# Optimization experiments

Hardware: AMD Instinct MI355X
Metric: run time of the kernel (lower is better)

## Reference

```python
import jax, jax.numpy as jnp
import numpy as np

WS = 7   # window_size
NH = 4   # num_head
EPS = 1e-5

def _rel_idx(ws):
    c = np.stack(np.meshgrid(np.arange(ws), np.arange(ws), indexing='ij')).reshape(2, -1)
    r = (c[:, :, None] - c[:, None, :]).transpose(1, 2, 0)
    r[..., 0] += ws - 1
    r[..., 1] += ws - 1
    r[..., 0] *= 2 * ws - 1
    return r.sum(-1)  # (ws^2, ws^2) int

def _shift_mask(ws, ps):
    # faithful to torch get_shift_mask: additive mask value is (1-eq)*1e-9 (as in source)
    wn = ps // ws
    ss = ws // 2
    rt = (np.arange(ps) + ss) // ws
    m = rt[:, None] * (ps // ws) + rt[None, :] + 1
    m = np.roll(m, (-ss, -ss), axis=(0, 1))
    m = m.reshape(wn, ws, wn, ws).transpose(0, 2, 1, 3).reshape(wn * wn, ws * ws)
    eq = (m[:, :, None] == m[:, None, :]).astype(np.float32)
    return (1.0 - eq) * 1e-9  # (num_windows, ws^2, ws^2)

def _ln(x, g, b):
    mu = x.mean(-1, keepdims=True)
    v = ((x - mu) ** 2).mean(-1, keepdims=True)
    return (x - mu) * jax.lax.rsqrt(v + EPS) * g + b

def _win_attn(x, wqkv, bqkv, wo, bo, table, mask):
    bs, S, D = x.shape
    hd = D // NH
    qkv = x @ wqkv.T + bqkv
    q, k, v = jnp.split(qkv, 3, axis=-1)
    def heads(t):
        return t.reshape(bs, S, NH, hd).transpose(0, 2, 1, 3).reshape(bs * NH, S, hd)
    q, k, v = heads(q), heads(k), heads(v)
    ridx = _rel_idx(WS).reshape(-1)
    bias = table[ridx].reshape(S, S, NH).transpose(2, 0, 1)  # (NH, S, S)
    scores = jnp.einsum('bqd,bkd->bqk', q, k) / np.sqrt(hd).astype(np.float32)
    scores = scores + jnp.tile(bias, (bs, 1, 1))
    if mask is not None:
        # source tiles mask head-major while q/k/v are batch-major; replicate faithfully
        scores = scores + jnp.tile(mask, (NH, 1, 1))
    p = jax.nn.softmax(scores, axis=-1)
    out = jnp.einsum('bqk,bkd->bqd', p, v)
    out = out.reshape(bs, NH, S, hd).transpose(0, 2, 1, 3).reshape(bs, S, D)
    return out @ wo.T + bo

def _forward(x, ln1_g, ln1_b, w_qkv1, b_qkv1, w_o1, b_o1, tbl1,
             ln2_g, ln2_b, w_mlp1, b_mlp1,
             ln3_g, ln3_b, w_qkv2, b_qkv2, w_o2, b_o2, tbl2,
             ln4_g, ln4_b, w_mlp2, b_mlp2):
    B, S, D = x.shape
    ps = int(np.sqrt(S))
    wn = ps // WS
    nw = wn * wn
    s2 = WS * WS
    ss = WS // 2
    # block 1: W-MSA (note: source's image2sequence is a plain reshape, no inverse transpose)
    y = _ln(x, ln1_g, ln1_b)
    y = y.reshape(B, wn, WS, wn, WS, D).transpose(0, 1, 3, 2, 4, 5).reshape(B * nw, s2, D)
    y = _win_attn(y, w_qkv1, b_qkv1, w_o1, b_o1, tbl1, None)
    y = y.reshape(B, S, D)
    x = x + y
    # mlp1
    y = _ln(x, ln2_g, ln2_b) @ w_mlp1.T + b_mlp1
    x = x + y
    # block 2: SW-MSA
    y = _ln(x, ln3_g, ln3_b)
    y = jnp.roll(y.reshape(B, ps, ps, D), (-ss, -ss), axis=(1, 2))
    y = y.reshape(B, wn, WS, wn, WS, D).transpose(0, 1, 3, 2, 4, 5).reshape(B * nw, s2, D)
    mask = jnp.tile(jnp.asarray(_shift_mask(WS, ps)), (B, 1, 1))
    y = _win_attn(y, w_qkv2, b_qkv2, w_o2, b_o2, tbl2, mask)
    y = y.reshape(B, wn, wn, WS, WS, D).transpose(0, 1, 3, 2, 4, 5).reshape(B, ps, ps, D)
    y = jnp.roll(y, (ss, ss), axis=(1, 2)).reshape(B, S, D)
    x = x + y
    # mlp2; source line `y + x + y` has no assignment, so the final residual is dropped
    y = _ln(x, ln4_g, ln4_b) @ w_mlp2.T + b_mlp2
    return y

def setup_inputs() -> dict:
    key = jax.random.key(0)
    ks = jax.random.split(key, 16)
    B, S, D = 64, 3136, 128
    T = (2 * WS - 1) ** 2  # 169
    f32 = jnp.float32
    inp = {
        'x': jax.random.normal(ks[0], (B, S, D), dtype=f32),
        'ln1_g': jnp.ones((D,), f32), 'ln1_b': jnp.zeros((D,), f32),
        'w_qkv1': jax.random.normal(ks[1], (3 * D, D), dtype=f32) * 0.02,
        'b_qkv1': jnp.zeros((3 * D,), f32),
        'w_o1': jax.random.normal(ks[2], (D, D), dtype=f32) * 0.02,
        'b_o1': jnp.zeros((D,), f32),
        'tbl1': jax.random.normal(ks[3], (T, NH), dtype=f32) * 0.02,
        'ln2_g': jnp.ones((D,), f32), 'ln2_b': jnp.zeros((D,), f32),
        'w_mlp1': jax.random.normal(ks[4], (D, D), dtype=f32) * 0.02,
        'b_mlp1': jnp.zeros((D,), f32),
        'ln3_g': jnp.ones((D,), f32), 'ln3_b': jnp.zeros((D,), f32),
        'w_qkv2': jax.random.normal(ks[5], (3 * D, D), dtype=f32) * 0.02,
        'b_qkv2': jnp.zeros((3 * D,), f32),
        'w_o2': jax.random.normal(ks[6], (D, D), dtype=f32) * 0.02,
        'b_o2': jnp.zeros((D,), f32),
        'tbl2': jax.random.normal(ks[7], (T, NH), dtype=f32) * 0.02,
        'ln4_g': jnp.ones((D,), f32), 'ln4_b': jnp.zeros((D,), f32),
        'w_mlp2': jax.random.normal(ks[8], (D, D), dtype=f32) * 0.02,
        'b_mlp2': jnp.zeros((D,), f32),
    }
    return inp

def reference(x, ln1_g, ln1_b, w_qkv1, b_qkv1, w_o1, b_o1, tbl1,
              ln2_g, ln2_b, w_mlp1, b_mlp1,
              ln3_g, ln3_b, w_qkv2, b_qkv2, w_o2, b_o2, tbl2,
              ln4_g, ln4_b, w_mlp2, b_mlp2):
    return _forward(x, ln1_g, ln1_b, w_qkv1, b_qkv1, w_o1, b_o1, tbl1,
                    ln2_g, ln2_b, w_mlp1, b_mlp1,
                    ln3_g, ln3_b, w_qkv2, b_qkv2, w_o2, b_o2, tbl2,
                    ln4_g, ln4_b, w_mlp2, b_mlp2)
```

## Files before the change

### kernel.cpp

```cpp
#include <hip/hip_runtime.h>
#include <hip/hip_bf16.h>
#include <stdint.h>

#define PS 56
#define S_ 3136
#define DIM 128
#define NTOK 200704

typedef __attribute__((ext_vector_type(8))) short short8;
typedef __attribute__((ext_vector_type(4))) float f32x4;

__device__ __forceinline__ float bflo(uint32_t u){ return __uint_as_float(u << 16); }
__device__ __forceinline__ float bfhi(uint32_t u){ return __uint_as_float(u & 0xffff0000u); }
__device__ __forceinline__ uint32_t bfpack(float a, float b){
  uint32_t ua = __float_as_uint(a); ua = (ua + 0x7fffu + ((ua >> 16) & 1u)) >> 16;
  uint32_t ub = __float_as_uint(b); ub = (ub + 0x7fffu + ((ub >> 16) & 1u)) & 0xffff0000u;
  return ua | ub;
}
__device__ __forceinline__ uint16_t bf16of(float a){
  uint32_t ua = __float_as_uint(a);
  return (uint16_t)((ua + 0x7fffu + ((ua >> 16) & 1u)) >> 16);
}

__device__ __forceinline__ int win_map(int r, int shift) {
  int b = r / S_;
  int rem = r - b * S_;
  int w = rem / 49;
  int p = rem - w * 49;
  int i = p / 7, j = p - i * 7;
  int wr = w >> 3, wc = w & 7;
  int row = wr * 7 + i + shift; if (row >= PS) row -= PS;
  int col = wc * 7 + j + shift; if (col >= PS) col -= PS;
  return b * S_ + row * PS + col;
}

__global__ __launch_bounds__(256) void ln_k(const float* __restrict__ X,
                                            const float* __restrict__ g,
                                            const float* __restrict__ b,
                                            uint16_t* __restrict__ O) {
  int t = blockIdx.x * 4 + (threadIdx.x >> 6);
  int lane = threadIdx.x & 63;
  float2 v = *(const float2*)(X + (size_t)t * DIM + lane * 2);
  float s = v.x + v.y, sq = v.x * v.x + v.y * v.y;
  #pragma unroll
  for (int o = 32; o; o >>= 1) { s += __shfl_xor(s, o); sq += __shfl_xor(sq, o); }
  float mu = s * (1.0f / 128.0f);
  float rs = rsqrtf(sq * (1.0f / 128.0f) - mu * mu + 1e-5f);
  float2 gg = *(const float2*)(g + lane * 2);
  float2 bb = *(const float2*)(b + lane * 2);
  float a = (v.x - mu) * rs * gg.x + bb.x;
  float c = (v.y - mu) * rs * gg.y + bb.y;
  ((uint32_t*)O)[(size_t)t * 64 + lane] = bfpack(a, c);
}

__global__ __launch_bounds__(256) void wconv_k(
    const float* __restrict__ w0, const float* __restrict__ w1,
    const float* __restrict__ w2, const float* __restrict__ w3,
    const float* __restrict__ w4, const float* __restrict__ w5,
    uint16_t* __restrict__ out) {
  int i = blockIdx.x * 256 + threadIdx.x;
  float v;
  if      (i <  49152) v = w0[i];
  else if (i <  98304) v = w1[i -  49152];
  else if (i < 114688) v = w2[i -  98304];
  else if (i < 131072) v = w3[i - 114688];
  else if (i < 147456) v = w4[i - 131072];
  else                 v = w5[i - 147456];
  out[i] = bf16of(v);
}

constexpr int MKC = 64, MKSTR = MKC + 8;

template<int IN_SHIFT, int OUT_SHIFT, bool RES, bool OUT_BF16>
__global__ __launch_bounds__(256) void gemm_m2(
    const uint16_t* __restrict__ A, const uint16_t* __restrict__ Wb,
    const float* __restrict__ bias, const float* __restrict__ Rsrc,
    void* __restrict__ Out, int Ncols)
{
  __shared__ __align__(16) uint16_t As[128][MKSTR];
  __shared__ __align__(16) uint16_t Ws[128][MKSTR];
  const int tid = threadIdx.x;
  const int lane = tid & 63;
  const int lanelow = lane & 15;
  const int quad = lane >> 4;
  const int wid = tid >> 6;
  const int wave_m = wid >> 1, wave_n = wid & 1;
  const int mtile = blockIdx.y * 128;
  const int ntile = blockIdx.x * 128;

  f32x4 acc[4][4];
  #pragma unroll
  for (int mt = 0; mt < 4; ++mt)
    #pragma unroll
    for (int nt = 0; nt < 4; ++nt) acc[mt][nt] = (f32x4){0.f, 0.f, 0.f, 0.f};

  for (int kc = 0; kc < DIM; kc += MKC) {
    #pragma unroll
    for (int it = 0; it < 8; ++it) {
      int idx = tid + it * 256;
      int m = idx >> 4;
      int k4 = (idx & 15) << 2;
      int gm = mtile + m;
      int src = (IN_SHIFT < 0) ? gm : win_map(gm, IN_SHIFT);
      *(uint2*)&As[m][k4] = *(const uint2*)(A + (size_t)src * DIM + kc + k4);
    }
    #pragma unroll
    for (int it = 0; it < 8; ++it) {
      int idx = tid + it * 256;
      int n = idx >> 4;
      int k4 = (idx & 15) << 2;
      *(uint2*)&Ws[n][k4] = *(const uint2*)(Wb + (size_t)(ntile + n) * DIM + kc + k4);
    }
    __syncthreads();
    #pragma unroll
    for (int k0 = 0; k0 < MKC; k0 += 32) {
      short8 af[4], bf[4];
      #pragma unroll
      for (int mt = 0; mt < 4; ++mt)
        af[mt] = *(const short8*)&As[wave_m * 64 + mt * 16 + lanelow][k0 + quad * 8];
      #pragma unroll
      for (int nt = 0; nt < 4; ++nt)
        bf[nt] = *(const short8*)&Ws[wave_n * 64 + nt * 16 + lanelow][k0 + quad * 8];
      #pragma unroll
      for (int mt = 0; mt < 4; ++mt)
        #pragma unroll
        for (int nt = 0; nt < 4; ++nt)
          acc[mt][nt] = __builtin_amdgcn_mfma_f32_16x16x32_bf16(af[mt], bf[nt], acc[mt][nt], 0, 0, 0);
    }
    __syncthreads();
  }
  #pragma unroll
  for (int nt = 0; nt < 4; ++nt) {
    int col = ntile + wave_n * 64 + nt * 16 + lanelow;
    float bb = bias[col];
    #pragma unroll
    for (int mt = 0; mt < 4; ++mt) {
      #pragma unroll
      for (int r = 0; r < 4; ++r) {
        int gm = mtile + wave_m * 64 + mt * 16 + quad * 4 + r;
        float v = acc[mt][nt][r] + bb;
        if constexpr (OUT_BF16) {
          ((uint16_t*)Out)[(size_t)gm * Ncols + col] = bf16of(v);
        } else {
          int orow = (OUT_SHIFT < 0) ? gm : win_map(gm, OUT_SHIFT);
          if constexpr (RES) v += Rsrc[(size_t)orow * DIM + col];
          ((float*)Out)[(size_t)orow * (size_t)Ncols + col] = v;
        }
      }
    }
  }
}

__global__ __launch_bounds__(256) void gemm_m3(
    const uint16_t* __restrict__ A, const uint16_t* __restrict__ Wb,
    const float* __restrict__ bias, const float* __restrict__ Rsrc,
    float* __restrict__ Xout, const float* __restrict__ lng,
    const float* __restrict__ lnb, uint16_t* __restrict__ xb)
{
  __shared__ __align__(16) uint16_t As[128][MKSTR];
  __shared__ __align__(16) uint16_t Ws[128][MKSTR];
  __shared__ float lnred[128][2][2];
  const int tid = threadIdx.x;
  const int lane = tid & 63;
  const int lanelow = lane & 15;
  const int quad = lane >> 4;
  const int wid = tid >> 6;
  const int wave_m = wid >> 1, wave_n = wid & 1;
  const int mtile = blockIdx.y * 128;

  f32x4 acc[4][4];
  #pragma unroll
  for (int mt = 0; mt < 4; ++mt)
    #pragma unroll
    for (int nt = 0; nt < 4; ++nt) acc[mt][nt] = (f32x4){0.f, 0.f, 0.f, 0.f};

  for (int kc = 0; kc < DIM; kc += MKC) {
    #pragma unroll
    for (int it = 0; it < 8; ++it) {
      int idx = tid + it * 256;
      int m = idx >> 4;
      int k4 = (idx & 15) << 2;
      *(uint2*)&As[m][k4] = *(const uint2*)(A + (size_t)(mtile + m) * DIM + kc + k4);
    }
    #pragma unroll
    for (int it = 0; it < 8; ++it) {
      int idx = tid + it * 256;
      int n = idx >> 4;
      int k4 = (idx & 15) << 2;
      *(uint2*)&Ws[n][k4] = *(const uint2*)(Wb + (size_t)n * DIM + kc + k4);
    }
    __syncthreads();
    #pragma unroll
    for (int k0 = 0; k0 < MKC; k0 += 32) {
      short8 af[4], bf[4];
      #pragma unroll
      for (int mt = 0; mt < 4; ++mt)
        af[mt] = *(const short8*)&As[wave_m * 64 + mt * 16 + lanelow][k0 + quad * 8];
      #pragma unroll
      for (int nt = 0; nt < 4; ++nt)
        bf[nt] = *(const short8*)&Ws[wave_n * 64 + nt * 16 + lanelow][k0 + quad * 8];
      #pragma unroll
      for (int mt = 0; mt < 4; ++mt)
        #pragma unroll
        for (int nt = 0; nt < 4; ++nt)
          acc[mt][nt] = __builtin_amdgcn_mfma_f32_16x16x32_bf16(af[mt], bf[nt], acc[mt][nt], 0, 0, 0);
    }
    __syncthreads();
  }
  float bb[4], gg[4], bt[4];
  #pragma unroll
  for (int nt = 0; nt < 4; ++nt) {
    int col = wave_n * 64 + nt * 16 + lanelow;
    bb[nt] = bias[col]; gg[nt] = lng[col]; bt[nt] = lnb[col];
  }
  #pragma unroll
  for (int mt = 0; mt < 4; ++mt)
    #pragma unroll
    for (int r = 0; r < 4; ++r) {
      int gm = mtile + wave_m * 64 + mt * 16 + quad * 4 + r;
      float s = 0.f, sq = 0.f;
      #pragma unroll
      for (int nt = 0; nt < 4; ++nt) {
        int col = wave_n * 64 + nt * 16 + lanelow;
        float v = acc[mt][nt][r] + bb[nt] + Rsrc[(size_t)gm * DIM + col];
        acc[mt][nt][r] = v;
        s += v; sq += v * v;
      }
      s += __shfl_xor(s, 1); sq += __shfl_xor(sq, 1);
      s += __shfl_xor(s, 2); sq += __shfl_xor(sq, 2);
      s += __shfl_xor(s, 4); sq += __shfl_xor(sq, 4);
      s += __shfl_xor(s, 8); sq += __shfl_xor(sq, 8);
      if (lanelow == 0) {
        int lr = wave_m * 64 + mt * 16 + quad * 4 + r;
        lnred[lr][wave_n][0] = s;
        lnred[lr][wave_n][1] = sq;
      }
    }
  __syncthreads();
  #pragma unroll
  for (int mt = 0; mt < 4; ++mt)
    #pragma unroll
    for (int r = 0; r < 4; ++r) {
      int lr = wave_m * 64 + mt * 16 + quad * 4 + r;
      int gm = mtile + lr;
      float s  = lnred[lr][0][0] + lnred[lr][1][0];
      float sq = lnred[lr][0][1] + lnred[lr][1][1];
      float mu = s * (1.0f / 128.0f);
      float rs = rsqrtf(sq * (1.0f / 128.0f) - mu * mu + 1e-5f);
      #pragma unroll
      for (int nt = 0; nt < 4; ++nt) {
        int col = wave_n * 64 + nt * 16 + lanelow;
        float v = acc[mt][nt][r];
        Xout[(size_t)gm * DIM + col] = v;
        xb[(size_t)gm * DIM + col] = bf16of((v - mu) * rs * gg[nt] + bt[nt]);
      }
    }
}

__global__ __launch_bounds__(256) void bias_k(const float* __restrict__ tbl, float* __restrict__ biasT) {
  int idx = blockIdx.x * 256 + threadIdx.x;
  int h = idx >> 12;
  int k = (idx >> 6) & 63;
  int q = idx & 63;
  float v;
  if (k >= 49)      v = -1e30f;
  else if (q >= 49) v = 0.f;
  else {
    int yi = q / 7, xi = q - yi * 7;
    int yj = k / 7, xj = k - yj * 7;
    v = tbl[((yi - yj + 6) * 13 + (xi - xj + 6)) * 4 + h];
  }
  biasT[idx] = v;
}

constexpr int QKV_STR = 392;
constexpr int OS_STR  = 140;

template<int IN_SHIFT, int OUT_SHIFT>
__global__ __launch_bounds__(256) void attn3(const uint16_t* __restrict__ xbin,
                                             const uint16_t* __restrict__ Wqkv,
                                             const float* __restrict__ bqkv,
                                             const float* __restrict__ biasT,
                                             const uint16_t* __restrict__ Wo,
                                             const float* __restrict__ bo,
                                             const float* __restrict__ Rsrc,
                                             float* __restrict__ Xout,
                                             const float* __restrict__ lng,
                                             const float* __restrict__ lnb,
                                             uint16_t* __restrict__ xbout)
{
  __shared__ __align__(16) uint16_t qs[64 * QKV_STR];
  __shared__ float lnred[64][4][2];
  const int tid = threadIdx.x;
  const int lane = tid & 63;
  const int h = tid >> 6;
  const int lanelow = lane & 15;
  const int quad = lane >> 4;
  const int base = blockIdx.x * 49;

  {
    short8 af[4][4];
    #pragma unroll
    for (int mt = 0; mt < 4; ++mt) {
      int tok = mt * 16 + lanelow; if (tok > 48) tok = 48;
      int src = win_map(base + tok, IN_SHIFT);
      const uint16_t* arow = xbin + (size_t)src * DIM;
      #pragma unroll
      for (int k0 = 0; k0 < 4; ++k0)
        af[mt][k0] = *(const short8*)(arow + k0 * 32 + quad * 8);
    }
    #pragma unroll
    for (int ntl = 0; ntl < 6; ++ntl) {
      int wrow = (ntl >> 1) * 128 + h * 32 + (ntl & 1) * 16 + lanelow;
      const uint16_t* wr_ = Wqkv + (size_t)wrow * DIM;
      short8 bfr[4];
      #pragma unroll
      for (int k0 = 0; k0 < 4; ++k0)
        bfr[k0] = *(const short8*)(wr_ + k0 * 32 + quad * 8);
      f32x4 a4[4];
      #pragma unroll
      for (int mt = 0; mt < 4; ++mt) a4[mt] = (f32x4){0.f, 0.f, 0.f, 0.f};
      #pragma unroll
      for (int k0 = 0; k0 < 4; ++k0)
        #pragma unroll
        for (int mt = 0; mt < 4; ++mt)
          a4[mt] = __builtin_amdgcn_mfma_f32_16x16x32_bf16(af[mt][k0], bfr[k0], a4[mt], 0, 0, 0);
      float bq = bqkv[wrow];
      #pragma unroll
      for (int mt = 0; mt < 4; ++mt)
        #pragma unroll
        for (int r = 0; r < 4; ++r)
          qs[(mt * 16 + quad * 4 + r) * QKV_STR + wrow] = bf16of(a4[mt][r] + bq);
    }
  }

  const int n0 = h * 32 + lanelow, n1 = n0 + 16;
  int   orow_a[4][4];
  float r0a[4][4], r1a[4][4];
  #pragma unroll
  for (int qt = 0; qt < 4; ++qt)
    #pragma unroll
    for (int r = 0; r < 4; ++r) {
      int q = qt * 16 + quad * 4 + r;
      bool ok = (q < 49);
      int wrow = base + (ok ? q : 0);
      int orow = (OUT_SHIFT < 0) ? wrow : win_map(wrow, OUT_SHIFT);
      orow_a[qt][r] = orow;
      r0a[qt][r] = ok ? Rsrc[(size_t)orow * DIM + n0] : 0.f;
      r1a[qt][r] = ok ? Rsrc[(size_t)orow * DIM + n1] : 0.f;
    }

  f32x4 sc[4][4];
  #pragma unroll
  for (int kt = 0; kt < 4; ++kt)
    #pragma unroll
    for (int qt = 0; qt < 4; ++qt) sc[kt][qt] = (f32x4){0.f, 0.f, 0.f, 0.f};
  {
    short8 kf[4], qf[4];
    const int kcol = 128 + h * 32 + quad * 8;
    const int qcol = h * 32 + quad * 8;
    #pragma unroll
    for (int t = 0; t < 4; ++t) {
      int tok = t * 16 + lanelow; if (tok > 48) tok = 48;
      kf[t] = *(const short8*)(qs + tok * QKV_STR + kcol);
      qf[t] = *(const short8*)(qs + tok * QKV_STR + qcol);
    }
    __syncthreads();
    #pragma unroll
    for (int kt = 0; kt < 4; ++kt)
      #pragma unroll
      for (int qt = 0; qt < 4; ++qt)
        sc[kt][qt] = __builtin_amdgcn_mfma_f32_16x16x32_bf16(kf[kt], qf[qt], sc[kt][qt], 0, 0, 0);
  }

  const float* bh = biasT + h * 4096;
  #pragma unroll
  for (int kt = 0; kt < 4; ++kt)
    #pragma unroll
    for (int r = 0; r < 4; ++r) {
      const float* br = bh + (kt * 16 + quad * 4 + r) * 64 + lanelow;
      #pragma unroll
      for (int qt = 0; qt < 4; ++qt)
        sc[kt][qt][r] = fmaf(sc[kt][qt][r], 0.17677669529663689f, br[qt * 16]);
    }
  #pragma unroll
  for (int qt = 0; qt < 4; ++qt) {
    float m = sc[0][qt][0];
    #pragma unroll
    for (int kt = 0; kt < 4; ++kt)
      #pragma unroll
      for (int r = 0; r < 4; ++r) m = fmaxf(m, sc[kt][qt][r]);
    m = fmaxf(m, __shfl_xor(m, 16));
    m = fmaxf(m, __shfl_xor(m, 32));
    float s = 0.f;
    #pragma unroll
    for (int kt = 0; kt < 4; ++kt)
      #pragma unroll
      for (int r = 0; r < 4; ++r) {
        float e = __expf(sc[kt][qt][r] - m);
        sc[kt][qt][r] = e;
        s += e;
      }
    s += __shfl_xor(s, 16);
    s += __shfl_xor(s, 32);
    float inv = 1.0f / s;
    #pragma unroll
    for (int kt = 0; kt < 4; ++kt)
      #pragma unroll
      for (int r = 0; r < 4; ++r) sc[kt][qt][r] *= inv;
  }

  uint16_t* pw = qs + h * 64;
  #pragma unroll
  for (int qt = 0; qt < 4; ++qt)
    #pragma unroll
    for (int kt = 0; kt < 4; ++kt) {
      uint2 pk;
      pk.x = bfpack(sc[kt][qt][0], sc[kt][qt][1]);
      pk.y = bfpack(sc[kt][qt][2], sc[kt][qt][3]);
      *(uint2*)(pw + (qt * 16 + lanelow) * QKV_STR + kt * 16 + quad * 4) = pk;
    }

  f32x4 oc[4][2];
  #pragma unroll
  for (int qt = 0; qt < 4; ++qt)
    #pragma unroll
    for (int dt = 0; dt < 2; ++dt) oc[qt][dt] = (f32x4){0.f, 0.f, 0.f, 0.f};
  {
    short8 pf[4][2];
    #pragma unroll
    for (int qt = 0; qt < 4; ++qt)
      #pragma unroll
      for (int kp = 0; kp < 2; ++kp)
        pf[qt][kp] = *(const short8*)(pw + (qt * 16 + lanelow) * QKV_STR + kp * 32 + quad * 8);
    short8 vf[2][2];
    #pragma unroll
    for (int dt = 0; dt < 2; ++dt)
      #pragma unroll
      for (int kp = 0; kp < 2; ++kp) {
        short8 b;
        #pragma unroll
        for (int j = 0; j < 8; ++j) {
          int tok = kp * 32 + quad * 8 + j; if (tok > 48) tok = 48;
          b[j] = (short)qs[tok * QKV_STR + 256 + h * 32 + dt * 16 + lanelow];
        }
        vf[dt][kp] = b;
      }
    #pragma unroll
    for (int qt = 0; qt < 4; ++qt)
      #pragma unroll
      for (int dt = 0; dt < 2; ++dt)
        #pragma unroll
        for (int kp = 0; kp < 2; ++kp)
          oc[qt][dt] = __builtin_amdgcn_mfma_f32_16x16x32_bf16(pf[qt][kp], vf[dt][kp], oc[qt][dt], 0, 0, 0);
  }

  __syncthreads();
  uint16_t* Os = qs;
  #pragma unroll
  for (int qt = 0; qt < 4; ++qt)
    #pragma unroll
    for (int r = 0; r < 4; ++r) {
      int t = qt * 16 + quad * 4 + r;
      #pragma unroll
      for (int dt = 0; dt < 2; ++dt)
        Os[t * OS_STR + h * 32 + dt * 16 + lanelow] = bf16of(oc[qt][dt][r]);
    }
  __syncthreads();

  f32x4 rc[4][2];
  #pragma unroll
  for (int qt = 0; qt < 4; ++qt)
    #pragma unroll
    for (int dt = 0; dt < 2; ++dt) rc[qt][dt] = (f32x4){0.f, 0.f, 0.f, 0.f};
  #pragma unroll
  for (int kp = 0; kp < 4; ++kp) {
    short8 af[4];
    #pragma unroll
    for (int qt = 0; qt < 4; ++qt)
      af[qt] = *(const short8*)&Os[(qt * 16 + lanelow) * OS_STR + kp * 32 + quad * 8];
    short8 bfr[2];
    #pragma unroll
    for (int dt = 0; dt < 2; ++dt)
      bfr[dt] = *(const short8*)(Wo + (size_t)(h * 32 + dt * 16 + lanelow) * DIM + kp * 32 + quad * 8);
    #pragma unroll
    for (int qt = 0; qt < 4; ++qt)
      #pragma unroll
      for (int dt = 0; dt < 2; ++dt)
        rc[qt][dt] = __builtin_amdgcn_mfma_f32_16x16x32_bf16(af[qt], bfr[dt], rc[qt][dt], 0, 0, 0);
  }

  const float b0 = bo[n0], b1 = bo[n1];
  const float g0 = lng[n0], g1 = lng[n1];
  const float e0 = lnb[n0], e1 = lnb[n1];
  #pragma unroll
  for (int qt = 0; qt < 4; ++qt)
    #pragma unroll
    for (int r = 0; r < 4; ++r) {
      int q = qt * 16 + quad * 4 + r;
      float v0 = rc[qt][0][r] + b0 + r0a[qt][r];
      float v1 = rc[qt][1][r] + b1 + r1a[qt][r];
      rc[qt][0][r] = v0; rc[qt][1][r] = v1;
      float s = v0 + v1, sq = v0 * v0 + v1 * v1;
      s += __shfl_xor(s, 1); sq += __shfl_xor(sq, 1);
      s += __shfl_xor(s, 2); sq += __shfl_xor(sq, 2);
      s += __shfl_xor(s, 4); sq += __shfl_xor(sq, 4);
      s += __shfl_xor(s, 8); sq += __shfl_xor(sq, 8);
      if (lanelow == 0) { lnred[q][h][0] = s; lnred[q][h][1] = sq; }
    }
  __syncthreads();
  #pragma unroll
  for (int qt = 0; qt < 4; ++qt)
    #pragma unroll
    for (int r = 0; r < 4; ++r) {
      int q = qt * 16 + quad * 4 + r;
      if (q < 49) {
        int orow = orow_a[qt][r];
        float s  = lnred[q][0][0] + lnred[q][1][0] + lnred[q][2][0] + lnred[q][3][0];
        float sq = lnred[q][0][1] + lnred[q][1][1] + lnred[q][2][1] + lnred[q][3][1];
        float mu = s * (1.0f / 128.0f);
        float rs = rsqrtf(sq * (1.0f / 128.0f) - mu * mu + 1e-5f);
        float v0 = rc[qt][0][r], v1 = rc[qt][1][r];
        Xout[(size_t)orow * DIM + n0] = v0;
        Xout[(size_t)orow * DIM + n1] = v1;
        xbout[(size_t)orow * DIM + n0] = bf16of((v0 - mu) * rs * g0 + e0);
        xbout[(size_t)orow * DIM + n1] = bf16of((v1 - mu) * rs * g1 + e1);
      }
    }
}

extern "C" void kernel_launch(void* const* d_in, const int* in_sizes, int n_in,
                              void* d_out, int out_size, void* d_ws, size_t ws_size,
                              hipStream_t stream) {
  const float* x0    = (const float*)d_in[0];
  const float* ln1g  = (const float*)d_in[1];
  const float* ln1b  = (const float*)d_in[2];
  const float* wqkv1 = (const float*)d_in[3];
  const float* bqkv1 = (const float*)d_in[4];
  const float* wo1   = (const float*)d_in[5];
  const float* bo1   = (const float*)d_in[6];
  const float* tbl1  = (const float*)d_in[7];
  const float* ln2g  = (const float*)d_in[8];
  const float* ln2b  = (const float*)d_in[9];
  const float* wm1   = (const float*)d_in[10];
  const float* bm1   = (const float*)d_in[11];
  const float* ln3g  = (const float*)d_in[12];
  const float* ln3b  = (const float*)d_in[13];
  const float* wqkv2 = (const float*)d_in[14];
  const float* bqkv2 = (const float*)d_in[15];
  const float* wo2   = (const float*)d_in[16];
  const float* bo2   = (const float*)d_in[17];
  const float* tbl2  = (const float*)d_in[18];
  const float* ln4g  = (const float*)d_in[19];
  const float* ln4b  = (const float*)d_in[20];
  const float* wm2   = (const float*)d_in[21];
  const float* bm2   = (const float*)d_in[22];

  char* ws = (char*)d_ws;
  size_t off = 0;
  uint16_t* xbA  = (uint16_t*)(ws + off); off += (size_t)NTOK * 128 * sizeof(uint16_t);
  uint16_t* xb2  = (uint16_t*)(ws + off); off += (size_t)NTOK * 128 * sizeof(uint16_t);
  float* biasT1  = (float*)(ws + off);    off += 16384 * sizeof(float);
  float* biasT2  = (float*)(ws + off);    off += 16384 * sizeof(float);
  uint16_t* wb   = (uint16_t*)(ws + off); off += 163840 * sizeof(uint16_t);
  if (ws_size < off) return;
  float* x1 = (float*)d_out;

  uint16_t* wqkv1b = wb;
  uint16_t* wqkv2b = wb + 49152;
  uint16_t* wo1b   = wb + 98304;
  uint16_t* wm1b   = wb + 114688;
  uint16_t* wo2b   = wb + 131072;
  uint16_t* wm2b   = wb + 147456;

  dim3 blk(256);
  dim3 lgrid(NTOK / 4);
  dim3 g1m(1, 1568);
  dim3 agrid(4096);

  wconv_k<<<640, blk, 0, stream>>>(wqkv1, wqkv2, wo1, wm1, wo2, wm2, wb);
  bias_k<<<64, blk, 0, stream>>>(tbl1, biasT1);
  bias_k<<<64, blk, 0, stream>>>(tbl2, biasT2);

  ln_k<<<lgrid, blk, 0, stream>>>(x0, ln1g, ln1b, xbA);
  attn3<0, -1><<<agrid, blk, 0, stream>>>(xbA, wqkv1b, bqkv1, biasT1, wo1b, bo1,
                                          x0, x1, ln2g, ln2b, xb2);
  gemm_m3<<<g1m, blk, 0, stream>>>(xb2, wm1b, bm1, x1, x1, ln3g, ln3b, xbA);
  attn3<3, 3><<<agrid, blk, 0, stream>>>(xbA, wqkv2b, bqkv2, biasT2, wo2b, bo2,
                                         x1, x1, ln4g, ln4b, xb2);
  gemm_m2<-1, -1, false, false><<<g1m, blk, 0, stream>>>(xb2, wm2b, bm2, nullptr, d_out, 128);
}
```

Before: 711.0 us.

## Use direct-register MLP GEMM and transposed V layout in window attention

Replaces the LDS-staged 128x128 MLP GEMMs with a 64-row kernel that loads A and W fragments straight from global memory into registers, with the LayerNorm epilogue kept optional. In the attention kernel, Q/K are written with packed vector stores via a swapped-operand MFMA, and V is stored transposed in its own shared buffer so V fragments become single 16-byte loads instead of eight scalar gathers. The aim is to cut LDS traffic, barriers and scalar shared-memory accesses. In exchange the GEMM gets no W reuse through LDS, and the attention kernel needs more shared memory.

Result: no change. 698.1 us (-1.8%).

```diff
diff --git a/kernel.cpp b/kernel.cpp
--- a/kernel.cpp
+++ b/kernel.cpp
@@ -10,8 +10,6 @@
 typedef __attribute__((ext_vector_type(8))) short short8;
 typedef __attribute__((ext_vector_type(4))) float f32x4;
 
-__device__ __forceinline__ float bflo(uint32_t u){ return __uint_as_float(u << 16); }
-__device__ __forceinline__ float bfhi(uint32_t u){ return __uint_as_float(u & 0xffff0000u); }
 __device__ __forceinline__ uint32_t bfpack(float a, float b){
   uint32_t ua = __float_as_uint(a); ua = (ua + 0x7fffu + ((ua >> 16) & 1u)) >> 16;
   uint32_t ub = __float_as_uint(b); ub = (ub + 0x7fffu + ((ub >> 16) & 1u)) & 0xffff0000u;
@@ -69,192 +67,96 @@
   out[i] = bf16of(v);
 }
 
-constexpr int MKC = 64, MKSTR = MKC + 8;
-
-template<int IN_SHIFT, int OUT_SHIFT, bool RES, bool OUT_BF16>
-__global__ __launch_bounds__(256) void gemm_m2(
+template<bool RES, bool DOLN>
+__global__ __launch_bounds__(256) void gemm_d(
     const uint16_t* __restrict__ A, const uint16_t* __restrict__ Wb,
     const float* __restrict__ bias, const float* __restrict__ Rsrc,
-    void* __restrict__ Out, int Ncols)
+    float* __restrict__ Xout, const float* __restrict__ lng,
+    const float* __restrict__ lnb, uint16_t* __restrict__ xbout)
 {
-  __shared__ __align__(16) uint16_t As[128][MKSTR];
-  __shared__ __align__(16) uint16_t Ws[128][MKSTR];
+  __shared__ float lnred[64][4][2];
   const int tid = threadIdx.x;
   const int lane = tid & 63;
   const int lanelow = lane & 15;
   const int quad = lane >> 4;
-  const int wid = tid >> 6;
-  const int wave_m = wid >> 1, wave_n = wid & 1;
-  const int mtile = blockIdx.y * 128;
-  const int ntile = blockIdx.x * 128;
-
-  f32x4 acc[4][4];
+  const int w = tid >> 6;
+  const int base = blockIdx.x * 64;
+
+  short8 af[4][4];
+  #pragma unroll
+  for (int mt = 0; mt < 4; ++mt) {
+    const uint16_t* arow = A + (size_t)(base + mt * 16 + lanelow) * DIM;
+    #pragma unroll
+    for (int k0 = 0; k0 < 4; ++k0)
+      af[mt][k0] = *(const short8*)(arow + k0 * 32 + quad * 8);
+  }
+  f32x4 acc[4][2];
   #pragma unroll
   for (int mt = 0; mt < 4; ++mt)
     #pragma unroll
-    for (int nt = 0; nt < 4; ++nt) acc[mt][nt] = (f32x4){0.f, 0.f, 0.f, 0.f};
-
-  for (int kc = 0; kc < DIM; kc += MKC) {
-    #pragma unroll
-    for (int it = 0; it < 8; ++it) {
-      int idx = tid + it * 256;
-      int m = idx >> 4;
-      int k4 = (idx & 15) << 2;
-      int gm = mtile + m;
-      int src = (IN_SHIFT < 0) ? gm : win_map(gm, IN_SHIFT);
-      *(uint2*)&As[m][k4] = *(const uint2*)(A + (size_t)src * DIM + kc + k4);
-    }
-    #pragma unroll
-    for (int it = 0; it < 8; ++it) {
-      int idx = tid + it * 256;
-      int n = idx >> 4;
-      int k4 = (idx & 15) << 2;
-      *(uint2*)&Ws[n][k4] = *(const uint2*)(Wb + (size_t)(ntile + n) * DIM + kc + k4);
-    }
+    for (int nt = 0; nt < 2; ++nt) acc[mt][nt] = (f32x4){0.f, 0.f, 0.f, 0.f};
+  #pragma unroll
+  for (int nt = 0; nt < 2; ++nt) {
+    int wrow = w * 32 + nt * 16 + lanelow;
+    const uint16_t* wr_ = Wb + (size_t)wrow * DIM;
+    short8 bfr[4];
+    #pragma unroll
+    for (int k0 = 0; k0 < 4; ++k0)
+      bfr[k0] = *(const short8*)(wr_ + k0 * 32 + quad * 8);
+    #pragma unroll
+    for (int k0 = 0; k0 < 4; ++k0)
+      #pragma unroll
+      for (int mt = 0; mt < 4; ++mt)
+        acc[mt][nt] = __builtin_amdgcn_mfma_f32_16x16x32_bf16(af[mt][k0], bfr[k0], acc[mt][nt], 0, 0, 0);
+  }
+  const int n0 = w * 32 + lanelow, n1 = n0 + 16;
+  const float b0 = bias[n0], b1 = bias[n1];
+  float g0, g1, e0, e1;
+  if constexpr (DOLN) { g0 = lng[n0]; g1 = lng[n1]; e0 = lnb[n0]; e1 = lnb[n1]; }
+  #pragma unroll
+  for (int mt = 0; mt < 4; ++mt)
+    #pragma unroll
+    for (int r = 0; r < 4; ++r) {
+      int row = mt * 16 + quad * 4 + r;
+      int gm = base + row;
+      float v0 = acc[mt][0][r] + b0;
+      float v1 = acc[mt][1][r] + b1;
+      if constexpr (RES) {
+        v0 += Rsrc[(size_t)gm * DIM + n0];
+        v1 += Rsrc[(size_t)gm * DIM + n1];
+      }
+      acc[mt][0][r] = v0; acc[mt][1][r] = v1;
+      if constexpr (DOLN) {
+        float s = v0 + v1, sq = v0 * v0 + v1 * v1;
+        s += __shfl_xor(s, 1); sq += __shfl_xor(sq, 1);
+        s += __shfl_xor(s, 2); sq += __shfl_xor(sq, 2);
+        s += __shfl_xor(s, 4); sq += __shfl_xor(sq, 4);
+        s += __shfl_xor(s, 8); sq += __shfl_xor(sq, 8);
+        if (lanelow == 0) { lnred[row][w][0] = s; lnred[row][w][1] = sq; }
+      } else {
+        Xout[(size_t)gm * DIM + n0] = v0;
+        Xout[(size_t)gm * DIM + n1] = v1;
+      }
+    }
+  if constexpr (DOLN) {
     __syncthreads();
     #pragma unroll
-    for (int k0 = 0; k0 < MKC; k0 += 32) {
-      short8 af[4], bf[4];
-      #pragma unroll
-      for (int mt = 0; mt < 4; ++mt)
-        af[mt] = *(const short8*)&As[wave_m * 64 + mt * 16 + lanelow][k0 + quad * 8];
-      #pragma unroll
-      for (int nt = 0; nt < 4; ++nt)
-        bf[nt] = *(const short8*)&Ws[wave_n * 64 + nt * 16 + lanelow][k0 + quad * 8];
-      #pragma unroll
-      for (int mt = 0; mt < 4; ++mt)
-        #pragma unroll
-        for (int nt = 0; nt < 4; ++nt)
-          acc[mt][nt] = __builtin_amdgcn_mfma_f32_16x16x32_bf16(af[mt], bf[nt], acc[mt][nt], 0, 0, 0);
-    }
-    __syncthreads();
-  }
-  #pragma unroll
-  for (int nt = 0; nt < 4; ++nt) {
-    int col = ntile + wave_n * 64 + nt * 16 + lanelow;
-    float bb = bias[col];
-    #pragma unroll
-    for (int mt = 0; mt < 4; ++mt) {
+    for (int mt = 0; mt < 4; ++mt)
       #pragma unroll
       for (int r = 0; r < 4; ++r) {
-        int gm = mtile + wave_m * 64 + mt * 16 + quad * 4 + r;
-        float v = acc[mt][nt][r] + bb;
-        if constexpr (OUT_BF16) {
-          ((uint16_t*)Out)[(size_t)gm * Ncols + col] = bf16of(v);
-        } else {
-          int orow = (OUT_SHIFT < 0) ? gm : win_map(gm, OUT_SHIFT);
-          if constexpr (RES) v += Rsrc[(size_t)orow * DIM + col];
-          ((float*)Out)[(size_t)orow * (size_t)Ncols + col] = v;
-        }
-      }
-    }
-  }
-}
-
-__global__ __launch_bounds__(256) void gemm_m3(
-    const uint16_t* __restrict__ A, const uint16_t* __restrict__ Wb,
-    const float* __restrict__ bias, const float* __restrict__ Rsrc,
-    float* __restrict__ Xout, const float* __restrict__ lng,
-    const float* __restrict__ lnb, uint16_t* __restrict__ xb)
-{
-  __shared__ __align__(16) uint16_t As[128][MKSTR];
-  __shared__ __align__(16) uint16_t Ws[128][MKSTR];
-  __shared__ float lnred[128][2][2];
-  const int tid = threadIdx.x;
-  const int lane = tid & 63;
-  const int lanelow = lane & 15;
-  const int quad = lane >> 4;
-  const int wid = tid >> 6;
-  const int wave_m = wid >> 1, wave_n = wid & 1;
-  const int mtile = blockIdx.y * 128;
-
-  f32x4 acc[4][4];
-  #pragma unroll
-  for (int mt = 0; mt < 4; ++mt)
-    #pragma unroll
-    for (int nt = 0; nt < 4; ++nt) acc[mt][nt] = (f32x4){0.f, 0.f, 0.f, 0.f};
-
-  for (int kc = 0; kc < DIM; kc += MKC) {
-    #pragma unroll
-    for (int it = 0; it < 8; ++it) {
-      int idx = tid + it * 256;
-      int m = idx >> 4;
-      int k4 = (idx & 15) << 2;
-      *(uint2*)&As[m][k4] = *(const uint2*)(A + (size_t)(mtile + m) * DIM + kc + k4);
-    }
-    #pragma unroll
-    for (int it = 0; it < 8; ++it) {
-      int idx = tid + it * 256;
-      int n = idx >> 4;
-      int k4 = (idx & 15) << 2;
-      *(uint2*)&Ws[n][k4] = *(const uint2*)(Wb + (size_t)n * DIM + kc + k4);
-    }
-    __syncthreads();
-    #pragma unroll
-    for (int k0 = 0; k0 < MKC; k0 += 32) {
-      short8 af[4], bf[4];
-      #pragma unroll
-      for (int mt = 0; mt < 4; ++mt)
-        af[mt] = *(const short8*)&As[wave_m * 64 + mt * 16 + lanelow][k0 + quad * 8];
-      #pragma unroll
-      for (int nt = 0; nt < 4; ++nt)
-        bf[nt] = *(const short8*)&Ws[wave_n * 64 + nt * 16 + lanelow][k0 + quad * 8];
-      #pragma unroll
-      for (int mt = 0; mt < 4; ++mt)
-        #pragma unroll
-        for (int nt = 0; nt < 4; ++nt)
-          acc[mt][nt] = __builtin_amdgcn_mfma_f32_16x16x32_bf16(af[mt], bf[nt], acc[mt][nt], 0, 0, 0);
-    }
-    __syncthreads();
-  }
-  float bb[4], gg[4], bt[4];
-  #pragma unroll
-  for (int nt = 0; nt < 4; ++nt) {
-    int col = wave_n * 64 + nt * 16 + lanelow;
-    bb[nt] = bias[col]; gg[nt] = lng[col]; bt[nt] = lnb[col];
-  }
-  #pragma unroll
-  for (int mt = 0; mt < 4; ++mt)
-    #pragma unroll
-    for (int r = 0; r < 4; ++r) {
-      int gm = mtile + wave_m * 64 + mt * 16 + quad * 4 + r;
-      float s = 0.f, sq = 0.f;
-      #pragma unroll
-      for (int nt = 0; nt < 4; ++nt) {
-        int col = wave_n * 64 + nt * 16 + lanelow;
-        float v = acc[mt][nt][r] + bb[nt] + Rsrc[(size_t)gm * DIM + col];
-        acc[mt][nt][r] = v;
-        s += v; sq += v * v;
-      }
-      s += __shfl_xor(s, 1); sq += __shfl_xor(sq, 1);
-      s += __shfl_xor(s, 2); sq += __shfl_xor(sq, 2);
-      s += __shfl_xor(s, 4); sq += __shfl_xor(sq, 4);
-      s += __shfl_xor(s, 8); sq += __shfl_xor(sq, 8);
-      if (lanelow == 0) {
-        int lr = wave_m * 64 + mt * 16 + quad * 4 + r;
-        lnred[lr][wave_n][0] = s;
-        lnred[lr][wave_n][1] = sq;
-      }
-    }
-  __syncthreads();
-  #pragma unroll
-  for (int mt = 0; mt < 4; ++mt)
-    #pragma unroll
-    for (int r = 0; r < 4; ++r) {
-      int lr = wave_m * 64 + mt * 16 + quad * 4 + r;
-      int gm = mtile + lr;
-      float s  = lnred[lr][0][0] + lnred[lr][1][0];
-      float sq = lnred[lr][0][1] + lnred[lr][1][1];
-      float mu = s * (1.0f / 128.0f);
-      float rs = rsqrtf(sq * (1.0f / 128.0f) - mu * mu + 1e-5f);
-      #pragma unroll
-      for (int nt = 0; nt < 4; ++nt) {
-        int col = wave_n * 64 + nt * 16 + lanelow;
-        float v = acc[mt][nt][r];
-        Xout[(size_t)gm * DIM + col] = v;
-        xb[(size_t)gm * DIM + col] = bf16of((v - mu) * rs * gg[nt] + bt[nt]);
-      }
-    }
+        int row = mt * 16 + quad * 4 + r;
+        int gm = base + row;
+        float s  = lnred[row][0][0] + lnred[row][1][0] + lnred[row][2][0] + lnred[row][3][0];
+        float sq = lnred[row][0][1] + lnred[row][1][1] + lnred[row][2][1] + lnred[row][3][1];
+        float mu = s * (1.0f / 128.0f);
+        float rs = rsqrtf(sq * (1.0f / 128.0f) - mu * mu + 1e-5f);
+        float v0 = acc[mt][0][r], v1 = acc[mt][1][r];
+        Xout[(size_t)gm * DIM + n0] = v0;
+        Xout[(size_t)gm * DIM + n1] = v1;
+        xbout[(size_t)gm * DIM + n0] = bf16of((v0 - mu) * rs * g0 + e0);
+        xbout[(size_t)gm * DIM + n1] = bf16of((v1 - mu) * rs * g1 + e1);
+      }
+  }
 }
 
 __global__ __launch_bounds__(256) void bias_k(const float* __restrict__ tbl, float* __restrict__ biasT) {
@@ -273,8 +175,9 @@
   biasT[idx] = v;
 }
 
-constexpr int QKV_STR = 392;
-constexpr int OS_STR  = 140;
+constexpr int QKSTR = 264;
+constexpr int VSTR  = 72;
+constexpr int OS_STR = 140;
 
 template<int IN_SHIFT, int OUT_SHIFT>
 __global__ __launch_bounds__(256) void attn3(const uint16_t* __restrict__ xbin,
@@ -289,7 +192,8 @@
                                              const float* __restrict__ lnb,
                                              uint16_t* __restrict__ xbout)
 {
-  __shared__ __align__(16) uint16_t qs[64 * QKV_STR];
+  __shared__ __align__(16) uint16_t qk_s[64 * QKSTR];
+  __shared__ __align__(16) uint16_t vT[128 * VSTR];
   __shared__ float lnred[64][4][2];
   const int tid = threadIdx.x;
   const int lane = tid & 63;
@@ -310,8 +214,33 @@
         af[mt][k0] = *(const short8*)(arow + k0 * 32 + quad * 8);
     }
     #pragma unroll
-    for (int ntl = 0; ntl < 6; ++ntl) {
-      int wrow = (ntl >> 1) * 128 + h * 32 + (ntl & 1) * 16 + lanelow;
+    for (int ntl = 0; ntl < 4; ++ntl) {
+      int dbase = (ntl >> 1) * 128 + h * 32 + (ntl & 1) * 16;
+      const uint16_t* wr_ = Wqkv + (size_t)(dbase + lanelow) * DIM;
+      short8 bfr[4];
+      #pragma unroll
+      for (int k0 = 0; k0 < 4; ++k0)
+        bfr[k0] = *(const short8*)(wr_ + k0 * 32 + quad * 8);
+      f32x4 a4[4];
+      #pragma unroll
+      for (int mt = 0; mt < 4; ++mt) a4[mt] = (f32x4){0.f, 0.f, 0.f, 0.f};
+      #pragma unroll
+      for (int k0 = 0; k0 < 4; ++k0)
+        #pragma unroll
+        for (int mt = 0; mt < 4; ++mt)
+          a4[mt] = __builtin_amdgcn_mfma_f32_16x16x32_bf16(bfr[k0], af[mt][k0], a4[mt], 0, 0, 0);
+      float4 bq4 = *(const float4*)(bqkv + dbase + quad * 4);
+      #pragma unroll
+      for (int mt = 0; mt < 4; ++mt) {
+        uint2 pk;
+        pk.x = bfpack(a4[mt][0] + bq4.x, a4[mt][1] + bq4.y);
+        pk.y = bfpack(a4[mt][2] + bq4.z, a4[mt][3] + bq4.w);
+        *(uint2*)(qk_s + (mt * 16 + lanelow) * QKSTR + dbase + quad * 4) = pk;
+      }
+    }
+    #pragma unroll
+    for (int ntl = 0; ntl < 2; ++ntl) {
+      int wrow = 256 + h * 32 + ntl * 16 + lanelow;
       const uint16_t* wr_ = Wqkv + (size_t)wrow * DIM;
       short8 bfr[4];
       #pragma unroll
@@ -326,11 +255,14 @@
         for (int mt = 0; mt < 4; ++mt)
           a4[mt] = __builtin_amdgcn_mfma_f32_16x16x32_bf16(af[mt][k0], bfr[k0], a4[mt], 0, 0, 0);
       float bq = bqkv[wrow];
-      #pragma unroll
-      for (int mt = 0; mt < 4; ++mt)
-        #pragma unroll
-        for (int r = 0; r < 4; ++r)
-          qs[(mt * 16 + quad * 4 + r) * QKV_STR + wrow] = bf16of(a4[mt][r] + bq);
+      int vd = h * 32 + ntl * 16 + lanelow;
+      #pragma unroll
+      for (int mt = 0; mt < 4; ++mt) {
+        uint2 pk;
+        pk.x = bfpack(a4[mt][0] + bq, a4[mt][1] + bq);
+        pk.y = bfpack(a4[mt][2] + bq, a4[mt][3] + bq);
+        *(uint2*)(vT + (size_t)vd * VSTR + mt * 16 + quad * 4) = pk;
+      }
     }
   }
 
@@ -362,8 +294,8 @@
     #pragma unroll
     for (int t = 0; t < 4; ++t) {
       int tok = t * 16 + lanelow; if (tok > 48) tok = 48;
-      kf[t] = *(const short8*)(qs + tok * QKV_STR + kcol);
-      qf[t] = *(const short8*)(qs + tok * QKV_STR + qcol);
+      kf[t] = *(const short8*)(qk_s + tok * QKSTR + kcol);
+      qf[t] = *(const short8*)(qk_s + tok * QKSTR + qcol);
     }
     __syncthreads();
     #pragma unroll
@@ -410,7 +342,7 @@
       for (int r = 0; r < 4; ++r) sc[kt][qt][r] *= inv;
   }
 
-  uint16_t* pw = qs + h * 64;
+  uint16_t* pw = qk_s + h * 64;
   #pragma unroll
   for (int qt = 0; qt < 4; ++qt)
     #pragma unroll
@@ -418,7 +350,7 @@
       uint2 pk;
       pk.x = bfpack(sc[kt][qt][0], sc[kt][qt][1]);
       pk.y = bfpack(sc[kt][qt][2], sc[kt][qt][3]);
-      *(uint2*)(pw + (qt * 16 + lanelow) * QKV_STR + kt * 16 + quad * 4) = pk;
+      *(uint2*)(pw + (qt * 16 + lanelow) * QKSTR + kt * 16 + quad * 4) = pk;
     }
 
   f32x4 oc[4][2];
@@ -432,20 +364,13 @@
     for (int qt = 0; qt < 4; ++qt)
       #pragma unroll
       for (int kp = 0; kp < 2; ++kp)
-        pf[qt][kp] = *(const short8*)(pw + (qt * 16 + lanelow) * QKV_STR + kp * 32 + quad * 8);
+        pf[qt][kp] = *(const short8*)(pw + (qt * 16 + lanelow) * QKSTR + kp * 32 + quad * 8);
     short8 vf[2][2];
     #pragma unroll
     for (int dt = 0; dt < 2; ++dt)
       #pragma unroll
-      for (int kp = 0; kp < 2; ++kp) {
-        short8 b;
-        #pragma unroll
-        for (int j = 0; j < 8; ++j) {
-          int tok = kp * 32 + quad * 8 + j; if (tok > 48) tok = 48;
-          b[j] = (short)qs[tok * QKV_STR + 256 + h * 32 + dt * 16 + lanelow];
-        }
-        vf[dt][kp] = b;
-      }
+      for (int kp = 0; kp < 2; ++kp)
+        vf[dt][kp] = *(const short8*)(vT + (size_t)(h * 32 + dt * 16 + lanelow) * VSTR + kp * 32 + quad * 8);
     #pragma unroll
     for (int qt = 0; qt < 4; ++qt)
       #pragma unroll
@@ -456,7 +381,7 @@
   }
 
   __syncthreads();
-  uint16_t* Os = qs;
+  uint16_t* Os = qk_s;
   #pragma unroll
   for (int qt = 0; qt < 4; ++qt)
     #pragma unroll
@@ -575,7 +500,7 @@
 
   dim3 blk(256);
   dim3 lgrid(NTOK / 4);
-  dim3 g1m(1, 1568);
+  dim3 dgrid(NTOK / 64);
   dim3 agrid(4096);
 
   wconv_k<<<640, blk, 0, stream>>>(wqkv1, wqkv2, wo1, wm1, wo2, wm2, wb);
@@ -585,8 +510,9 @@
   ln_k<<<lgrid, blk, 0, stream>>>(x0, ln1g, ln1b, xbA);
   attn3<0, -1><<<agrid, blk, 0, stream>>>(xbA, wqkv1b, bqkv1, biasT1, wo1b, bo1,
                                           x0, x1, ln2g, ln2b, xb2);
-  gemm_m3<<<g1m, blk, 0, stream>>>(xb2, wm1b, bm1, x1, x1, ln3g, ln3b, xbA);
+  gemm_d<true, true><<<dgrid, blk, 0, stream>>>(xb2, wm1b, bm1, x1, x1, ln3g, ln3b, xbA);
   attn3<3, 3><<<agrid, blk, 0, stream>>>(xbA, wqkv2b, bqkv2, biasT2, wo2b, bo2,
                                          x1, x1, ln4g, ln4b, xb2);
-  gemm_m2<-1, -1, false, false><<<g1m, blk, 0, stream>>>(xb2, wm2b, bm2, nullptr, d_out, 128);
-}
+  gemm_d<false, false><<<dgrid, blk, 0, stream>>>(xb2, wm2b, bm2, nullptr, (float*)d_out,
+                                                  nullptr, nullptr, nullptr);
+}
```
